# Kernel tuning notes

Measured on AMD Instinct MI355X. Metric: run time of the kernel, lower is better.

Reference implementation:

```python
import jax, jax.numpy as jnp
import numpy as np

THETA = 10000.0
H, D_NOPE, D_ROPE, D_V = 12, 64, 64, 128
D_MODEL, D_LAT = 768, 128
B, S = 4, 2048


def _rope(x, pos, theta=THETA):
    # x: (B, S, D) with D even; pos: (S,) int. Matches RoPE.forward exactly
    # (interleaved even/odd rotation, freqs over full flattened D).
    D = x.shape[-1]
    inv_freq = 1.0 / theta ** (jnp.arange(0, D, 2, dtype=jnp.float32) / D)
    ang = pos.astype(jnp.float32)[:, None] * inv_freq        # (S, D/2)
    c, s = jnp.cos(ang), jnp.sin(ang)
    xe, xo = x[..., 0::2], x[..., 1::2]
    out = jnp.stack([xe * c - xo * s, xe * s + xo * c], axis=-1)
    return out.reshape(x.shape)


def setup_inputs() -> dict:
    key = jax.random.key(0)
    ks = jax.random.split(key, 12)
    std = 0.02
    inp = {
        'x': jax.random.normal(ks[0], (B, S, D_MODEL), jnp.float32),
        'token_positions': jnp.arange(S, dtype=jnp.int64) if jax.config.jax_enable_x64 else jnp.arange(S, dtype=jnp.int32),
        'W_dkv': jax.random.normal(ks[1], (D_LAT, D_MODEL), jnp.float32) * std,
        'b_dkv': jnp.zeros((D_LAT,), jnp.float32),
        'W_dq': jax.random.normal(ks[2], (D_LAT, D_MODEL), jnp.float32) * std,
        'b_dq': jnp.zeros((D_LAT,), jnp.float32),
        'W_uk_nope': jax.random.normal(ks[3], (H * D_NOPE, D_LAT), jnp.float32) * std,
        'b_uk_nope': jnp.zeros((H * D_NOPE,), jnp.float32),
        'W_uv': jax.random.normal(ks[4], (H * D_V, D_LAT), jnp.float32) * std,
        'b_uv': jnp.zeros((H * D_V,), jnp.float32),
        'W_uq_nope': jax.random.normal(ks[5], (H * D_NOPE, D_LAT), jnp.float32) * std,
        'b_uq_nope': jnp.zeros((H * D_NOPE,), jnp.float32),
        'W_uq_rope': jax.random.normal(ks[6], (H * D_ROPE, D_LAT), jnp.float32) * std,
        'b_uq_rope': jnp.zeros((H * D_ROPE,), jnp.float32),
        'W_uk_rope': jax.random.normal(ks[7], (H * D_ROPE, D_MODEL), jnp.float32) * std,
        'b_uk_rope': jnp.zeros((H * D_ROPE,), jnp.float32),
        'W_o': jax.random.normal(ks[8], (D_MODEL, H * D_V), jnp.float32) * std,
        'b_o': jnp.zeros((D_MODEL,), jnp.float32),
    }
    return inp


def reference(x, token_positions, W_dkv, b_dkv, W_dq, b_dq,
              W_uk_nope, b_uk_nope, W_uv, b_uv, W_uq_nope, b_uq_nope,
              W_uq_rope, b_uq_rope, W_uk_rope, b_uk_rope, W_o, b_o):
    b, s, _ = x.shape
    lin = lambda t, W, bb: t @ W.T + bb
    d_qk = D_NOPE + D_ROPE  # 128

    C_kv = lin(x, W_dkv, b_dkv)               # (B,S,128)
    C_q = lin(x, W_dq, b_dq)                  # (B,S,128)

    q_nope = lin(C_q, W_uq_nope, b_uq_nope)   # (B,S,H*64)
    k_nope = lin(C_kv, W_uk_nope, b_uk_nope)  # (B,S,H*64)
    v = lin(C_kv, W_uv, b_uv)                 # (B,S,H*128)

    q_rope = _rope(lin(C_q, W_uq_rope, b_uq_rope), token_positions)
    k_rope = _rope(lin(x, W_uk_rope, b_uk_rope), token_positions)

    # Faithful to torch: concat flattened nope||rope then view into heads.
    q = jnp.concatenate([q_nope, q_rope], axis=-1).reshape(b, s, H, d_qk).transpose(0, 2, 1, 3)
    k = jnp.concatenate([k_nope, k_rope], axis=-1).reshape(b, s, H, d_qk).transpose(0, 2, 1, 3)
    vh = v.reshape(b, s, H, D_V).transpose(0, 2, 1, 3)

    scale = 1.0 / jnp.sqrt(jnp.asarray(d_qk, x.dtype))
    logits = jnp.einsum('bhqd,bhkd->bhqk', q, k) * scale
    causal = jnp.tril(jnp.ones((s, s), bool))
    logits = jnp.where(causal, logits, jnp.finfo(logits.dtype).min)
    attn = jax.nn.softmax(logits, axis=-1)
    o = jnp.einsum('bhqk,bhkd->bhqd', attn, vh)      # (B,H,S,Dv)
    o = o.transpose(0, 2, 1, 3).reshape(b, s, H * D_V)
    return o @ W_o.T + b_o
```

## Files before the change

kernel.cpp:

```cpp
#include <hip/hip_runtime.h>

typedef __attribute__((ext_vector_type(8))) short short8;
typedef __attribute__((ext_vector_type(4))) short short4v;
typedef __attribute__((ext_vector_type(2))) int int2v;
typedef __attribute__((ext_vector_type(4))) float float4v;

#define MFMA16(a, b, c) __builtin_amdgcn_mfma_f32_16x16x32_bf16((a), (b), (c), 0, 0, 0)

__device__ __forceinline__ short f2bf(float f) {
  unsigned u = __float_as_uint(f);
  u += 0x7fffu + ((u >> 16) & 1u);
  return (short)(u >> 16);
}

__device__ __forceinline__ int pkbf(float a, float b) {
  return (int)(unsigned short)f2bf(a) | (((int)(unsigned short)f2bf(b)) << 16);
}

__device__ __forceinline__ int cvtpk(float a, float b) {
  int r;
  asm("v_cvt_pk_bf16_f32 %0, %1, %2" : "=v"(r) : "v"(a), "v"(b));
  return r;
}

__device__ __forceinline__ void glds16(const short* g, short* l) {
  __builtin_amdgcn_global_load_lds(
      (const __attribute__((address_space(1))) void*)g,
      (__attribute__((address_space(3))) void*)l, 16, 0, 0);
}

struct CastSeg { const float* src; short* dst; int n4; };
struct CastArgs { CastSeg seg[9]; int start[10]; };

__global__ __launch_bounds__(256) void castk(CastArgs a) {
  int blk = blockIdx.x;
  int si = 0;
#pragma unroll
  for (int i = 1; i < 9; i++) si += (blk >= a.start[i]);
  int i = (blk - a.start[si]) * 256 + threadIdx.x;
  if (i >= a.seg[si].n4) return;
  float4v f = ((const float4v*)a.seg[si].src)[i];
  short4v o;
  o[0] = f2bf(f[0]); o[1] = f2bf(f[1]); o[2] = f2bf(f[2]); o[3] = f2bf(f[3]);
  ((short4v*)a.seg[si].dst)[i] = o;
}

template <int ROPE, int OUTMODE, int SCALE>
__global__ __launch_bounds__(256, 2) void gemm_t(
    const short* __restrict__ A, int lda, const short* __restrict__ W, int ldw,
    const float* __restrict__ bias0, const float* __restrict__ bias1,
    int bsplit, int ropestart, void* __restrict__ outp, int ldo, int ocol,
    int K, const int* __restrict__ pos) {
  int tid = threadIdx.x, w = tid >> 6, lane = tid & 63;
  int quad = lane >> 4, l16 = lane & 15;
  int bm = blockIdx.y * 128, bn = blockIdx.x * 128;
  int wm = (w & 1) * 64, wn = (w >> 1) * 64;

  __shared__ short At[2][128 * 64];
  __shared__ short Bt[2][128 * 64];

  int srow[4], soff[4];
#pragma unroll
  for (int j = 0; j < 4; j++) {
    int r = w * 32 + j * 8 + (lane >> 3);
    srow[j] = r;
    soff[j] = ((lane & 7) ^ (r & 7)) << 3;
  }
  const short* Ag = A + (size_t)bm * lda;
  const short* Wg = W + (size_t)bn * ldw;

#pragma unroll
  for (int j = 0; j < 4; j++)
    glds16(Ag + (size_t)srow[j] * lda + soff[j], &At[0][(w * 32 + j * 8) * 64]);
#pragma unroll
  for (int j = 0; j < 4; j++)
    glds16(Wg + (size_t)srow[j] * ldw + soff[j], &Bt[0][(w * 32 + j * 8) * 64]);

  float4v acc[4][4];
  float4v z = {0.f, 0.f, 0.f, 0.f};
#pragma unroll
  for (int mi = 0; mi < 4; mi++)
#pragma unroll
    for (int ni = 0; ni < 4; ni++) acc[mi][ni] = z;

  int nk = K >> 6;
  for (int it = 0; it < nk; it++) {
    __syncthreads();
    if (it + 1 < nk) {
      int kt = (it + 1) << 6, nb = (it + 1) & 1;
#pragma unroll
      for (int j = 0; j < 4; j++)
        glds16(Ag + (size_t)srow[j] * lda + kt + soff[j],
               &At[nb][(w * 32 + j * 8) * 64]);
#pragma unroll
      for (int j = 0; j < 4; j++)
        glds16(Wg + (size_t)srow[j] * ldw + kt + soff[j],
               &Bt[nb][(w * 32 + j * 8) * 64]);
    }
    const short* Ab = At[it & 1];
    const short* Bb = Bt[it & 1];
#pragma unroll
    for (int ks = 0; ks < 2; ks++) {
      short8 af[4], bf[4];
#pragma unroll
      for (int mi = 0; mi < 4; mi++) {
        int row = wm + mi * 16 + l16;
        af[mi] = *(const short8*)&Ab[(row << 6) + ((((ks << 2) + quad) ^ (row & 7)) << 3)];
      }
#pragma unroll
      for (int ni = 0; ni < 4; ni++) {
        int row = wn + ni * 16 + l16;
        bf[ni] = *(const short8*)&Bb[(row << 6) + ((((ks << 2) + quad) ^ (row & 7)) << 3)];
      }
#pragma unroll
      for (int mi = 0; mi < 4; mi++)
#pragma unroll
        for (int ni = 0; ni < 4; ni++)
          acc[mi][ni] = MFMA16(af[mi], bf[ni], acc[mi][ni]);
    }
  }

#pragma unroll
  for (int ni = 0; ni < 4; ni++) {
    int col = bn + wn + ni * 16 + l16;
    float bv = (col < bsplit) ? bias0[col] : bias1[col - bsplit];
    float fr = 0.f;
    bool dorope = ROPE && (col >= ropestart);
    if (dorope) {
      int ri = (col - ropestart) & ~1;
      fr = exp2f((float)ri * (-13.287712379549449f / 768.0f));
    }
#pragma unroll
    for (int mi = 0; mi < 4; mi++) {
      int row0 = bm + wm + mi * 16 + quad * 4;
      if (OUTMODE == 2) {
        int bidx = row0 >> 11, s = row0 & 2047;
        short4v ov;
#pragma unroll
        for (int r = 0; r < 4; r++) ov[r] = f2bf(acc[mi][ni][r] + bv);
        *(short4v*)((short*)outp + ((size_t)(bidx * 1536 + col)) * 2048 + s) = ov;
      } else {
#pragma unroll
        for (int r = 0; r < 4; r++) {
          int row = row0 + r;
          float v = acc[mi][ni][r] + bv;
          if (ROPE) {
            float pv = __shfl_xor(v, 1, 64);
            if (dorope) {
              float ang = (float)pos[row & 2047] * fr;
              float sn, cs;
              __sincosf(ang, &sn, &cs);
              v = (col & 1) ? (pv * sn + v * cs) : (v * cs - pv * sn);
            }
          }
          if (SCALE) v *= 0.12751743f;
          if (OUTMODE == 1)
            ((float*)outp)[(size_t)row * ldo + ocol + col] = v;
          else
            ((short*)outp)[(size_t)row * ldo + ocol + col] = f2bf(v);
        }
      }
    }
  }
}

__global__ __launch_bounds__(256, 2) void mla_attn(const short* __restrict__ Q,
                                                   const short* __restrict__ K,
                                                   const short* __restrict__ Vt,
                                                   short* __restrict__ O) {
  const int ld = 1536, SEQ = 2048;
  int tid = threadIdx.x, w = tid >> 6, lane = tid & 63;
  int quad = lane >> 4, l16 = lane & 15;
  int o = (int)blockIdx.x;
  int rank = o / 48;
  int g = o - rank * 48;
  int qt = (15 - rank) * 128;
  int hh = g % 12, b = g / 12;
  int qw = qt + w * 32;

  __shared__ short Kt[2][64 * 128];
  __shared__ short Vl[2][128 * 64];
  __shared__ short Pm[4][32 * 64];
  short* pw = Pm[w];

  int kgo[4], vgo[4];
#pragma unroll
  for (int j = 0; j < 4; j++) {
    int rk = (w * 4 + j) * 4 + (lane >> 4);
    kgo[j] = rk * ld + (((lane & 15) ^ (rk & 7)) << 3);
    int rv = (w * 4 + j) * 8 + (lane >> 3);
    vgo[j] = rv * SEQ + (((lane & 7) ^ (rv & 7)) << 3);
  }
  const short* Kg = K + (size_t)b * SEQ * ld + hh * 128;
  const short* Vg = Vt + (size_t)(b * 12 + hh) * 128 * SEQ;

  short8 qf[2][4];
  {
    const short* Qg = Q + (size_t)(b * SEQ + qw + l16) * ld + hh * 128 + quad * 8;
#pragma unroll
    for (int nf = 0; nf < 2; nf++)
#pragma unroll
      for (int ks = 0; ks < 4; ks++)
        qf[nf][ks] = *(const short8*)(Qg + (size_t)nf * 16 * ld + ks * 32);
  }

  float4v z = {0.f, 0.f, 0.f, 0.f};
  float4v oacc[2][8];
#pragma unroll
  for (int mq = 0; mq < 2; mq++)
#pragma unroll
    for (int df = 0; df < 8; df++) oacc[mq][df] = z;
  float l_i[2] = {0.f, 0.f};

#pragma unroll
  for (int j = 0; j < 4; j++) glds16(Kg + kgo[j], &Kt[0][(w * 4 + j) * 512]);
#pragma unroll
  for (int j = 0; j < 4; j++) glds16(Vg + vgo[j], &Vl[0][(w * 4 + j) * 512]);

  int ntiles = (qt >> 6) + 2;
  for (int it = 0; it < ntiles; it++) {
    int kt = it << 6;
    __syncthreads();
    if (it + 1 < ntiles) {
      int nb = (it + 1) & 1;
      const short* kn = Kg + (size_t)(kt + 64) * ld;
      const short* vn = Vg + (kt + 64);
#pragma unroll
      for (int j = 0; j < 4; j++) glds16(kn + kgo[j], &Kt[nb][(w * 4 + j) * 512]);
#pragma unroll
      for (int j = 0; j < 4; j++) glds16(vn + vgo[j], &Vl[nb][(w * 4 + j) * 512]);
    }
    if (kt > qw + 31) continue;
    const short* Kb = Kt[it & 1];
    const short* Vb = Vl[it & 1];

    float4v sf[4][2];
#pragma unroll
    for (int mf = 0; mf < 4; mf++)
#pragma unroll
      for (int nf = 0; nf < 2; nf++) sf[mf][nf] = z;
    __builtin_amdgcn_s_setprio(1);
#pragma unroll
    for (int ks = 0; ks < 4; ks++)
#pragma unroll
      for (int mf = 0; mf < 4; mf++) {
        int row = mf * 16 + l16;
        short8 a = *(const short8*)&Kb[(row << 7) + (((ks * 4 + quad) ^ (row & 7)) << 3)];
#pragma unroll
        for (int nf = 0; nf < 2; nf++) sf[mf][nf] = MFMA16(a, qf[nf][ks], sf[mf][nf]);
      }
    __builtin_amdgcn_s_setprio(0);
    if (kt + 63 > qw) {
#pragma unroll
      for (int mf = 0; mf < 4; mf++) {
        int key = kt + mf * 16 + quad * 4;
#pragma unroll
        for (int nf = 0; nf < 2; nf++) {
          int q = qw + nf * 16 + l16;
#pragma unroll
          for (int r = 0; r < 4; r++)
            if (key + r > q) sf[mf][nf][r] = -3e38f;
        }
      }
    }
#pragma unroll
    for (int nf = 0; nf < 2; nf++) {
      float ps = 0.f;
#pragma unroll
      for (int mf = 0; mf < 4; mf++)
#pragma unroll
        for (int r = 0; r < 4; r++) {
          float e = exp2f(sf[mf][nf][r]);
          sf[mf][nf][r] = e;
          ps += e;
        }
      l_i[nf] += ps;
#pragma unroll
      for (int mf = 0; mf < 4; mf++) {
        int2v pk;
        pk[0] = cvtpk(sf[mf][nf][0], sf[mf][nf][1]);
        pk[1] = cvtpk(sf[mf][nf][2], sf[mf][nf][3]);
        int p = (mf * 2 + (quad >> 1)) ^ (l16 & 7);
        *(int2v*)&pw[((nf * 16 + l16) << 6) + (p << 3) + ((quad & 1) << 2)] = pk;
      }
    }
    __builtin_amdgcn_s_setprio(1);
#pragma unroll
    for (int t = 0; t < 2; t++) {
      short8 pf[2];
#pragma unroll
      for (int mq = 0; mq < 2; mq++)
        pf[mq] = *(const short8*)&pw[((mq * 16 + l16) << 6) +
                                     ((((t << 2) + quad) ^ (l16 & 7)) << 3)];
#pragma unroll
      for (int df = 0; df < 8; df++) {
        int vr = df * 16 + l16;
        short8 vf = *(const short8*)&Vb[(vr << 6) + ((((t << 2) + quad) ^ (vr & 7)) << 3)];
#pragma unroll
        for (int mq = 0; mq < 2; mq++) oacc[mq][df] = MFMA16(pf[mq], vf, oacc[mq][df]);
      }
    }
    __builtin_amdgcn_s_setprio(0);
  }

  short* Og = O + (size_t)(b * SEQ + qw) * ld + hh * 128;
#pragma unroll
  for (int mq = 0; mq < 2; mq++) {
    float l = l_i[mq];
    l += __shfl_xor(l, 16, 64);
    l += __shfl_xor(l, 32, 64);
    float linv = 1.0f / l;
    float lb[4];
#pragma unroll
    for (int r = 0; r < 4; r++) lb[r] = __shfl(linv, (quad << 2) + r, 64);
#pragma unroll
    for (int df = 0; df < 8; df++)
#pragma unroll
      for (int r = 0; r < 4; r++)
        Og[(size_t)(mq * 16 + (quad << 2) + r) * ld + df * 16 + l16] =
            f2bf(oacc[mq][df][r] * lb[r]);
  }
}

extern "C" void kernel_launch(void* const* d_in, const int* in_sizes, int n_in,
                              void* d_out, int out_size, void* d_ws, size_t ws_size,
                              hipStream_t stream) {
  const int S = 2048, DM = 768, DL = 128, HD = 1536;
  const int M = 4 * S;
  const int BIG = 1 << 28;

  const float* x = (const float*)d_in[0];
  const int* pos = (const int*)d_in[1];
  const float* W_dkv = (const float*)d_in[2];
  const float* b_dkv = (const float*)d_in[3];
  const float* W_dq = (const float*)d_in[4];
  const float* b_dq = (const float*)d_in[5];
  const float* W_uk_nope = (const float*)d_in[6];
  const float* b_uk_nope = (const float*)d_in[7];
  const float* W_uv = (const float*)d_in[8];
  const float* b_uv = (const float*)d_in[9];
  const float* W_uq_nope = (const float*)d_in[10];
  const float* b_uq_nope = (const float*)d_in[11];
  const float* W_uq_rope = (const float*)d_in[12];
  const float* b_uq_rope = (const float*)d_in[13];
  const float* W_uk_rope = (const float*)d_in[14];
  const float* b_uk_rope = (const float*)d_in[15];
  const float* W_o = (const float*)d_in[16];
  const float* b_o = (const float*)d_in[17];

  char* p = (char*)d_ws;
  size_t off = 0;
  auto take = [&](size_t nelem) -> short* {
    short* r = (short*)(p + off);
    off += (nelem * 2 + 255) & ~(size_t)255;
    return r;
  };
  short* xb = take((size_t)M * DM);
  short* Wdq = take(DL * DM);
  short* Wdkv = take(DL * DM);
  short* Wuqnope = take(768 * DL);
  short* Wuqrope = take(768 * DL);
  short* Wuknope = take(768 * DL);
  short* Wuv = take(1536 * DL);
  short* Wukrope = take(768 * DM);
  short* Wo = take(768 * 1536);
  short* Cm = take((size_t)M * 256);
  short* Qm = take((size_t)M * HD);
  short* Km = take((size_t)M * HD);
  short* Vtm = take((size_t)M * HD);
  short* Om = take((size_t)M * HD);
  if (off > ws_size) return;

  CastArgs ca;
  const float* srcs[9] = {x, W_dq, W_dkv, W_uq_nope, W_uq_rope, W_uk_nope, W_uv, W_uk_rope, W_o};
  short* dsts[9] = {xb, Wdq, Wdkv, Wuqnope, Wuqrope, Wuknope, Wuv, Wukrope, Wo};
  int ns[9] = {M * DM, DL * DM, DL * DM, 768 * DL, 768 * DL, 768 * DL, 1536 * DL, 768 * DM, 768 * 1536};
  ca.start[0] = 0;
  for (int i = 0; i < 9; i++) {
    ca.seg[i].src = srcs[i];
    ca.seg[i].dst = dsts[i];
    ca.seg[i].n4 = ns[i] / 4;
    ca.start[i + 1] = ca.start[i] + (ca.seg[i].n4 + 255) / 256;
  }
  castk<<<dim3(ca.start[9]), dim3(256), 0, stream>>>(ca);

  gemm_t<0, 0, 0><<<dim3(2, M / 128), dim3(256), 0, stream>>>(
      xb, DM, Wdq, DM, b_dq, b_dkv, 128, 0, Cm, 256, 0, DM, pos);
  gemm_t<1, 0, 1><<<dim3(12, M / 128), dim3(256), 0, stream>>>(
      Cm, 256, Wuqnope, DL, b_uq_nope, b_uq_rope, 768, 768, Qm, HD, 0, DL, pos);
  gemm_t<0, 0, 0><<<dim3(6, M / 128), dim3(256), 0, stream>>>(
      Cm + 128, 256, Wuknope, DL, b_uk_nope, b_uk_nope, BIG, 0, Km, HD, 0, DL, pos);
  gemm_t<1, 0, 0><<<dim3(6, M / 128), dim3(256), 0, stream>>>(
      xb, DM, Wukrope, DM, b_uk_rope, b_uk_rope, BIG, 0, Km, HD, 768, DM, pos);
  gemm_t<0, 2, 0><<<dim3(12, M / 128), dim3(256), 0, stream>>>(
      Cm + 128, 256, Wuv, DL, b_uv, b_uv, BIG, 0, Vtm, 0, 0, DL, pos);
  mla_attn<<<dim3(768), dim3(256), 0, stream>>>(Qm, Km, Vtm, Om);
  gemm_t<0, 1, 0><<<dim3(6, M / 128), dim3(256), 0, stream>>>(
      Om, HD, Wo, HD, b_o, b_o, BIG, 0, d_out, 768, 0, HD, pos);
}
```

Baseline: 326.5 us.

## Batch projection GEMMs into grouped launches and unroll attention tile loop

Replaces the templated GEMM with a runtime-dispatched grouped GEMM, so independent projections share one launch each: down-projections plus k_rope, and q/k_nope/v up-projections. For K=128 it loads both K tiles up front and syncs once. The attention loop is unrolled by two with static buffer indices and precomputed LDS byte offsets. The aim is fewer launches, better wave fill and less address arithmetic, at the cost of runtime flag branches and higher register pressure in the epilogue.

```diff
diff --git a/kernel.cpp b/kernel.cpp
--- a/kernel.cpp
+++ b/kernel.cpp
@@ -11,10 +11,6 @@
   unsigned u = __float_as_uint(f);
   u += 0x7fffu + ((u >> 16) & 1u);
   return (short)(u >> 16);
-}
-
-__device__ __forceinline__ int pkbf(float a, float b) {
-  return (int)(unsigned short)f2bf(a) | (((int)(unsigned short)f2bf(b)) << 16);
 }
 
 __device__ __forceinline__ int cvtpk(float a, float b) {
@@ -45,16 +41,25 @@
   ((short4v*)a.seg[si].dst)[i] = o;
 }
 
-template <int ROPE, int OUTMODE, int SCALE>
-__global__ __launch_bounds__(256, 2) void gemm_t(
-    const short* __restrict__ A, int lda, const short* __restrict__ W, int ldw,
-    const float* __restrict__ bias0, const float* __restrict__ bias1,
-    int bsplit, int ropestart, void* __restrict__ outp, int ldo, int ocol,
-    int K, const int* __restrict__ pos) {
+struct GSeg {
+  const short* A;
+  const short* W;
+  const float* bias0;
+  const float* bias1;
+  void* outp;
+  int lda, ldw, bsplit, ropestart, ldo, ocol, K, flags;
+};
+struct GArgs { GSeg s[3]; int start[4]; };
+
+__global__ __launch_bounds__(256, 2) void gemm_rt(GArgs ga, const int* __restrict__ pos) {
+  int bx = blockIdx.x;
+  int si = (bx >= ga.start[1]) + (bx >= ga.start[2]);
+  const GSeg sg = ga.s[si];
   int tid = threadIdx.x, w = tid >> 6, lane = tid & 63;
   int quad = lane >> 4, l16 = lane & 15;
-  int bm = blockIdx.y * 128, bn = blockIdx.x * 128;
+  int bm = blockIdx.y * 128, bn = (bx - ga.start[si]) * 128;
   int wm = (w & 1) * 64, wn = (w >> 1) * 64;
+  int lda = sg.lda, ldw = sg.ldw;
 
   __shared__ short At[2][128 * 64];
   __shared__ short Bt[2][128 * 64];
@@ -66,15 +71,8 @@
     srow[j] = r;
     soff[j] = ((lane & 7) ^ (r & 7)) << 3;
   }
-  const short* Ag = A + (size_t)bm * lda;
-  const short* Wg = W + (size_t)bn * ldw;
-
-#pragma unroll
-  for (int j = 0; j < 4; j++)
-    glds16(Ag + (size_t)srow[j] * lda + soff[j], &At[0][(w * 32 + j * 8) * 64]);
-#pragma unroll
-  for (int j = 0; j < 4; j++)
-    glds16(Wg + (size_t)srow[j] * ldw + soff[j], &Bt[0][(w * 32 + j * 8) * 64]);
+  const short* Ag = sg.A + (size_t)bm * lda;
+  const short* Wg = sg.W + (size_t)bn * ldw;
 
   float4v acc[4][4];
   float4v z = {0.f, 0.f, 0.f, 0.f};
@@ -83,22 +81,7 @@
 #pragma unroll
     for (int ni = 0; ni < 4; ni++) acc[mi][ni] = z;
 
-  int nk = K >> 6;
-  for (int it = 0; it < nk; it++) {
-    __syncthreads();
-    if (it + 1 < nk) {
-      int kt = (it + 1) << 6, nb = (it + 1) & 1;
-#pragma unroll
-      for (int j = 0; j < 4; j++)
-        glds16(Ag + (size_t)srow[j] * lda + kt + soff[j],
-               &At[nb][(w * 32 + j * 8) * 64]);
-#pragma unroll
-      for (int j = 0; j < 4; j++)
-        glds16(Wg + (size_t)srow[j] * ldw + kt + soff[j],
-               &Bt[nb][(w * 32 + j * 8) * 64]);
-    }
-    const short* Ab = At[it & 1];
-    const short* Bb = Bt[it & 1];
+  auto comp = [&](const short* Ab, const short* Bb) {
 #pragma unroll
     for (int ks = 0; ks < 2; ks++) {
       short8 af[4], bf[4];
@@ -118,33 +101,71 @@
         for (int ni = 0; ni < 4; ni++)
           acc[mi][ni] = MFMA16(af[mi], bf[ni], acc[mi][ni]);
     }
-  }
-
+  };
+
+  int nk = sg.K >> 6;
+  if (nk == 2) {
+#pragma unroll
+    for (int j = 0; j < 4; j++) {
+      glds16(Ag + (size_t)srow[j] * lda + soff[j], &At[0][(w * 32 + j * 8) * 64]);
+      glds16(Ag + (size_t)srow[j] * lda + 64 + soff[j], &At[1][(w * 32 + j * 8) * 64]);
+      glds16(Wg + (size_t)srow[j] * ldw + soff[j], &Bt[0][(w * 32 + j * 8) * 64]);
+      glds16(Wg + (size_t)srow[j] * ldw + 64 + soff[j], &Bt[1][(w * 32 + j * 8) * 64]);
+    }
+    __syncthreads();
+    comp(At[0], Bt[0]);
+    comp(At[1], Bt[1]);
+  } else {
+#pragma unroll
+    for (int j = 0; j < 4; j++)
+      glds16(Ag + (size_t)srow[j] * lda + soff[j], &At[0][(w * 32 + j * 8) * 64]);
+#pragma unroll
+    for (int j = 0; j < 4; j++)
+      glds16(Wg + (size_t)srow[j] * ldw + soff[j], &Bt[0][(w * 32 + j * 8) * 64]);
+    for (int it = 0; it < nk; it++) {
+      __syncthreads();
+      if (it + 1 < nk) {
+        int kt = (it + 1) << 6, nb = (it + 1) & 1;
+#pragma unroll
+        for (int j = 0; j < 4; j++)
+          glds16(Ag + (size_t)srow[j] * lda + kt + soff[j],
+                 &At[nb][(w * 32 + j * 8) * 64]);
+#pragma unroll
+        for (int j = 0; j < 4; j++)
+          glds16(Wg + (size_t)srow[j] * ldw + kt + soff[j],
+                 &Bt[nb][(w * 32 + j * 8) * 64]);
+      }
+      comp(At[it & 1], Bt[it & 1]);
+    }
+  }
+
+  bool ropeF = sg.flags & 1, scaleF = sg.flags & 2;
+  bool vtF = sg.flags & 4, f32F = sg.flags & 8;
 #pragma unroll
   for (int ni = 0; ni < 4; ni++) {
     int col = bn + wn + ni * 16 + l16;
-    float bv = (col < bsplit) ? bias0[col] : bias1[col - bsplit];
+    float bv = (col < sg.bsplit) ? sg.bias0[col] : sg.bias1[col - sg.bsplit];
     float fr = 0.f;
-    bool dorope = ROPE && (col >= ropestart);
+    bool dorope = ropeF && (col >= sg.ropestart);
     if (dorope) {
-      int ri = (col - ropestart) & ~1;
+      int ri = (col - sg.ropestart) & ~1;
       fr = exp2f((float)ri * (-13.287712379549449f / 768.0f));
     }
 #pragma unroll
     for (int mi = 0; mi < 4; mi++) {
       int row0 = bm + wm + mi * 16 + quad * 4;
-      if (OUTMODE == 2) {
+      if (vtF) {
         int bidx = row0 >> 11, s = row0 & 2047;
         short4v ov;
 #pragma unroll
         for (int r = 0; r < 4; r++) ov[r] = f2bf(acc[mi][ni][r] + bv);
-        *(short4v*)((short*)outp + ((size_t)(bidx * 1536 + col)) * 2048 + s) = ov;
+        *(short4v*)((short*)sg.outp + ((size_t)(bidx * 1536 + col)) * 2048 + s) = ov;
       } else {
 #pragma unroll
         for (int r = 0; r < 4; r++) {
           int row = row0 + r;
           float v = acc[mi][ni][r] + bv;
-          if (ROPE) {
+          if (ropeF) {
             float pv = __shfl_xor(v, 1, 64);
             if (dorope) {
               float ang = (float)pos[row & 2047] * fr;
@@ -153,11 +174,11 @@
               v = (col & 1) ? (pv * sn + v * cs) : (v * cs - pv * sn);
             }
           }
-          if (SCALE) v *= 0.12751743f;
-          if (OUTMODE == 1)
-            ((float*)outp)[(size_t)row * ldo + ocol + col] = v;
+          if (scaleF) v *= 0.12751743f;
+          if (f32F)
+            ((float*)sg.outp)[(size_t)row * sg.ldo + sg.ocol + col] = v;
           else
-            ((short*)outp)[(size_t)row * ldo + ocol + col] = f2bf(v);
+            ((short*)sg.outp)[(size_t)row * sg.ldo + sg.ocol + col] = f2bf(v);
         }
       }
     }
@@ -181,7 +202,7 @@
   __shared__ short Kt[2][64 * 128];
   __shared__ short Vl[2][128 * 64];
   __shared__ short Pm[4][32 * 64];
-  short* pw = Pm[w];
+  char* pwB = (char*)Pm[w];
 
   int kgo[4], vgo[4];
 #pragma unroll
@@ -204,6 +225,31 @@
         qf[nf][ks] = *(const short8*)(Qg + (size_t)nf * 16 * ld + ks * 32);
   }
 
+  int koff[4][4], voff[2][8], pfo[2][2], pwo[2][4];
+#pragma unroll
+  for (int ks = 0; ks < 4; ks++)
+#pragma unroll
+    for (int mf = 0; mf < 4; mf++) {
+      int row = mf * 16 + l16;
+      koff[ks][mf] = row * 256 + ((((ks << 2) + quad) ^ (row & 7)) << 4);
+    }
+#pragma unroll
+  for (int t = 0; t < 2; t++) {
+#pragma unroll
+    for (int df = 0; df < 8; df++) {
+      int vr = df * 16 + l16;
+      voff[t][df] = vr * 128 + ((((t << 2) + quad) ^ (vr & 7)) << 4);
+    }
+#pragma unroll
+    for (int mq = 0; mq < 2; mq++)
+      pfo[t][mq] = (mq * 16 + l16) * 128 + ((((t << 2) + quad) ^ (l16 & 7)) << 4);
+#pragma unroll
+    for (int mf = 0; mf < 4; mf++) {
+      int p = (mf * 2 + (quad >> 1)) ^ (l16 & 7);
+      pwo[t][mf] = (t * 16 + l16) * 128 + (p << 4) + ((quad & 1) << 3);
+    }
+  }
+
   float4v z = {0.f, 0.f, 0.f, 0.f};
   float4v oacc[2][8];
 #pragma unroll
@@ -218,90 +264,82 @@
   for (int j = 0; j < 4; j++) glds16(Vg + vgo[j], &Vl[0][(w * 4 + j) * 512]);
 
   int ntiles = (qt >> 6) + 2;
-  for (int it = 0; it < ntiles; it++) {
-    int kt = it << 6;
-    __syncthreads();
-    if (it + 1 < ntiles) {
-      int nb = (it + 1) & 1;
-      const short* kn = Kg + (size_t)(kt + 64) * ld;
-      const short* vn = Vg + (kt + 64);
-#pragma unroll
-      for (int j = 0; j < 4; j++) glds16(kn + kgo[j], &Kt[nb][(w * 4 + j) * 512]);
-#pragma unroll
-      for (int j = 0; j < 4; j++) glds16(vn + vgo[j], &Vl[nb][(w * 4 + j) * 512]);
-    }
-    if (kt > qw + 31) continue;
-    const short* Kb = Kt[it & 1];
-    const short* Vb = Vl[it & 1];
-
-    float4v sf[4][2];
-#pragma unroll
-    for (int mf = 0; mf < 4; mf++)
-#pragma unroll
-      for (int nf = 0; nf < 2; nf++) sf[mf][nf] = z;
-    __builtin_amdgcn_s_setprio(1);
-#pragma unroll
-    for (int ks = 0; ks < 4; ks++)
-#pragma unroll
-      for (int mf = 0; mf < 4; mf++) {
-        int row = mf * 16 + l16;
-        short8 a = *(const short8*)&Kb[(row << 7) + (((ks * 4 + quad) ^ (row & 7)) << 3)];
-#pragma unroll
-        for (int nf = 0; nf < 2; nf++) sf[mf][nf] = MFMA16(a, qf[nf][ks], sf[mf][nf]);
-      }
-    __builtin_amdgcn_s_setprio(0);
-    if (kt + 63 > qw) {
-#pragma unroll
-      for (int mf = 0; mf < 4; mf++) {
-        int key = kt + mf * 16 + quad * 4;
-#pragma unroll
-        for (int nf = 0; nf < 2; nf++) {
-          int q = qw + nf * 16 + l16;
-#pragma unroll
-          for (int r = 0; r < 4; r++)
-            if (key + r > q) sf[mf][nf][r] = -3e38f;
-        }
-      }
-    }
-#pragma unroll
-    for (int nf = 0; nf < 2; nf++) {
-      float ps = 0.f;
-#pragma unroll
-      for (int mf = 0; mf < 4; mf++)
-#pragma unroll
-        for (int r = 0; r < 4; r++) {
-          float e = exp2f(sf[mf][nf][r]);
-          sf[mf][nf][r] = e;
-          ps += e;
-        }
-      l_i[nf] += ps;
-#pragma unroll
-      for (int mf = 0; mf < 4; mf++) {
-        int2v pk;
-        pk[0] = cvtpk(sf[mf][nf][0], sf[mf][nf][1]);
-        pk[1] = cvtpk(sf[mf][nf][2], sf[mf][nf][3]);
-        int p = (mf * 2 + (quad >> 1)) ^ (l16 & 7);
-        *(int2v*)&pw[((nf * 16 + l16) << 6) + (p << 3) + ((quad & 1) << 2)] = pk;
-      }
-    }
-    __builtin_amdgcn_s_setprio(1);
-#pragma unroll
-    for (int t = 0; t < 2; t++) {
-      short8 pf[2];
-#pragma unroll
-      for (int mq = 0; mq < 2; mq++)
-        pf[mq] = *(const short8*)&pw[((mq * 16 + l16) << 6) +
-                                     ((((t << 2) + quad) ^ (l16 & 7)) << 3)];
-#pragma unroll
-      for (int df = 0; df < 8; df++) {
-        int vr = df * 16 + l16;
-        short8 vf = *(const short8*)&Vb[(vr << 6) + ((((t << 2) + quad) ^ (vr & 7)) << 3)];
-#pragma unroll
-        for (int mq = 0; mq < 2; mq++) oacc[mq][df] = MFMA16(pf[mq], vf, oacc[mq][df]);
-      }
-    }
-    __builtin_amdgcn_s_setprio(0);
-  }
+
+#define ATTN_TILE(IT, NB, NB1)                                                 \
+  do {                                                                         \
+    int kt = (IT) << 6;                                                        \
+    __syncthreads();                                                           \
+    if ((IT) + 1 < ntiles) {                                                   \
+      const short* kn = Kg + (size_t)(kt + 64) * ld;                           \
+      const short* vn = Vg + (kt + 64);                                        \
+      _Pragma("unroll") for (int j = 0; j < 4; j++)                            \
+          glds16(kn + kgo[j], &Kt[NB1][(w * 4 + j) * 512]);                    \
+      _Pragma("unroll") for (int j = 0; j < 4; j++)                            \
+          glds16(vn + vgo[j], &Vl[NB1][(w * 4 + j) * 512]);                    \
+    }                                                                          \
+    if (kt <= qw + 31) {                                                       \
+      const char* Kb = (const char*)Kt[NB];                                    \
+      const char* Vb = (const char*)Vl[NB];                                    \
+      float4v sf[4][2];                                                        \
+      __builtin_amdgcn_s_setprio(1);                                           \
+      _Pragma("unroll") for (int mf = 0; mf < 4; mf++) {                       \
+        short8 a = *(const short8*)(Kb + koff[0][mf]);                         \
+        sf[mf][0] = MFMA16(a, qf[0][0], z);                                    \
+        sf[mf][1] = MFMA16(a, qf[1][0], z);                                    \
+      }                                                                        \
+      _Pragma("unroll") for (int ks = 1; ks < 4; ks++) {                       \
+        _Pragma("unroll") for (int mf = 0; mf < 4; mf++) {                     \
+          short8 a = *(const short8*)(Kb + koff[ks][mf]);                      \
+          sf[mf][0] = MFMA16(a, qf[0][ks], sf[mf][0]);                         \
+          sf[mf][1] = MFMA16(a, qf[1][ks], sf[mf][1]);                         \
+        }                                                                      \
+      }                                                                        \
+      __builtin_amdgcn_s_setprio(0);                                           \
+      if (kt + 63 > qw) {                                                      \
+        _Pragma("unroll") for (int mf = 0; mf < 4; mf++) {                     \
+          int key = kt + mf * 16 + quad * 4;                                   \
+          _Pragma("unroll") for (int nf = 0; nf < 2; nf++) {                   \
+            int q = qw + nf * 16 + l16;                                        \
+            _Pragma("unroll") for (int r = 0; r < 4; r++)                      \
+                if (key + r > q) sf[mf][nf][r] = -3e38f;                       \
+          }                                                                    \
+        }                                                                      \
+      }                                                                        \
+      _Pragma("unroll") for (int nf = 0; nf < 2; nf++) {                       \
+        float ps = 0.f;                                                        \
+        _Pragma("unroll") for (int mf = 0; mf < 4; mf++)                       \
+            _Pragma("unroll") for (int r = 0; r < 4; r++) {                    \
+          float e = exp2f(sf[mf][nf][r]);                                      \
+          sf[mf][nf][r] = e;                                                   \
+          ps += e;                                                             \
+        }                                                                      \
+        l_i[nf] += ps;                                                         \
+        _Pragma("unroll") for (int mf = 0; mf < 4; mf++) {                     \
+          int2v pk;                                                            \
+          pk[0] = cvtpk(sf[mf][nf][0], sf[mf][nf][1]);                         \
+          pk[1] = cvtpk(sf[mf][nf][2], sf[mf][nf][3]);                         \
+          *(int2v*)(pwB + pwo[nf][mf]) = pk;                                   \
+        }                                                                      \
+      }                                                                        \
+      __builtin_amdgcn_s_setprio(1);                                           \
+      _Pragma("unroll") for (int t = 0; t < 2; t++) {                          \
+        short8 pf0 = *(const short8*)(pwB + pfo[t][0]);                        \
+        short8 pf1 = *(const short8*)(pwB + pfo[t][1]);                        \
+        _Pragma("unroll") for (int df = 0; df < 8; df++) {                     \
+          short8 vf = *(const short8*)(Vb + voff[t][df]);                      \
+          oacc[0][df] = MFMA16(pf0, vf, oacc[0][df]);                          \
+          oacc[1][df] = MFMA16(pf1, vf, oacc[1][df]);                          \
+        }                                                                      \
+      }                                                                        \
+      __builtin_amdgcn_s_setprio(0);                                           \
+    }                                                                          \
+  } while (0)
+
+  for (int it = 0; it < ntiles; it += 2) {
+    ATTN_TILE(it, 0, 1);
+    ATTN_TILE(it + 1, 1, 0);
+  }
+#undef ATTN_TILE
 
   short* Og = O + (size_t)(b * SEQ + qw) * ld + hh * 128;
 #pragma unroll
@@ -384,17 +422,38 @@
   }
   castk<<<dim3(ca.start[9]), dim3(256), 0, stream>>>(ca);
 
-  gemm_t<0, 0, 0><<<dim3(2, M / 128), dim3(256), 0, stream>>>(
-      xb, DM, Wdq, DM, b_dq, b_dkv, 128, 0, Cm, 256, 0, DM, pos);
-  gemm_t<1, 0, 1><<<dim3(12, M / 128), dim3(256), 0, stream>>>(
-      Cm, 256, Wuqnope, DL, b_uq_nope, b_uq_rope, 768, 768, Qm, HD, 0, DL, pos);
-  gemm_t<0, 0, 0><<<dim3(6, M / 128), dim3(256), 0, stream>>>(
-      Cm + 128, 256, Wuknope, DL, b_uk_nope, b_uk_nope, BIG, 0, Km, HD, 0, DL, pos);
-  gemm_t<1, 0, 0><<<dim3(6, M / 128), dim3(256), 0, stream>>>(
-      xb, DM, Wukrope, DM, b_uk_rope, b_uk_rope, BIG, 0, Km, HD, 768, DM, pos);
-  gemm_t<0, 2, 0><<<dim3(12, M / 128), dim3(256), 0, stream>>>(
-      Cm + 128, 256, Wuv, DL, b_uv, b_uv, BIG, 0, Vtm, 0, 0, DL, pos);
+  GArgs g1;
+  g1.s[0].A = xb;   g1.s[0].W = Wdq;      g1.s[0].bias0 = b_dq;      g1.s[0].bias1 = b_dkv;
+  g1.s[0].outp = Cm; g1.s[0].lda = DM; g1.s[0].ldw = DM; g1.s[0].bsplit = 128;
+  g1.s[0].ropestart = 0; g1.s[0].ldo = 256; g1.s[0].ocol = 0; g1.s[0].K = DM; g1.s[0].flags = 0;
+  g1.s[1].A = xb;   g1.s[1].W = Wukrope;  g1.s[1].bias0 = b_uk_rope; g1.s[1].bias1 = b_uk_rope;
+  g1.s[1].outp = Km; g1.s[1].lda = DM; g1.s[1].ldw = DM; g1.s[1].bsplit = BIG;
+  g1.s[1].ropestart = 0; g1.s[1].ldo = HD; g1.s[1].ocol = 768; g1.s[1].K = DM; g1.s[1].flags = 1;
+  g1.s[2] = g1.s[1];
+  g1.start[0] = 0; g1.start[1] = 2; g1.start[2] = 8; g1.start[3] = 8;
+  gemm_rt<<<dim3(8, M / 128), dim3(256), 0, stream>>>(g1, pos);
+
+  GArgs g2;
+  g2.s[0].A = Cm;   g2.s[0].W = Wuqnope;  g2.s[0].bias0 = b_uq_nope; g2.s[0].bias1 = b_uq_rope;
+  g2.s[0].outp = Qm; g2.s[0].lda = 256; g2.s[0].ldw = DL; g2.s[0].bsplit = 768;
+  g2.s[0].ropestart = 768; g2.s[0].ldo = HD; g2.s[0].ocol = 0; g2.s[0].K = DL; g2.s[0].flags = 1 | 2;
+  g2.s[1].A = Cm + 128; g2.s[1].W = Wuknope; g2.s[1].bias0 = b_uk_nope; g2.s[1].bias1 = b_uk_nope;
+  g2.s[1].outp = Km; g2.s[1].lda = 256; g2.s[1].ldw = DL; g2.s[1].bsplit = BIG;
+  g2.s[1].ropestart = 0; g2.s[1].ldo = HD; g2.s[1].ocol = 0; g2.s[1].K = DL; g2.s[1].flags = 0;
+  g2.s[2].A = Cm + 128; g2.s[2].W = Wuv;   g2.s[2].bias0 = b_uv;      g2.s[2].bias1 = b_uv;
+  g2.s[2].outp = Vtm; g2.s[2].lda = 256; g2.s[2].ldw = DL; g2.s[2].bsplit = BIG;
+  g2.s[2].ropestart = 0; g2.s[2].ldo = 0; g2.s[2].ocol = 0; g2.s[2].K = DL; g2.s[2].flags = 4;
+  g2.start[0] = 0; g2.start[1] = 12; g2.start[2] = 18; g2.start[3] = 30;
+  gemm_rt<<<dim3(30, M / 128), dim3(256), 0, stream>>>(g2, pos);
+
   mla_attn<<<dim3(768), dim3(256), 0, stream>>>(Qm, Km, Vtm, Om);
-  gemm_t<0, 1, 0><<<dim3(6, M / 128), dim3(256), 0, stream>>>(
-      Om, HD, Wo, HD, b_o, b_o, BIG, 0, d_out, 768, 0, HD, pos);
-}
+
+  GArgs g3;
+  g3.s[0].A = Om;   g3.s[0].W = Wo;       g3.s[0].bias0 = b_o;       g3.s[0].bias1 = b_o;
+  g3.s[0].outp = d_out; g3.s[0].lda = HD; g3.s[0].ldw = HD; g3.s[0].bsplit = BIG;
+  g3.s[0].ropestart = 0; g3.s[0].ldo = 768; g3.s[0].ocol = 0; g3.s[0].K = HD; g3.s[0].flags = 8;
+  g3.s[1] = g3.s[0];
+  g3.s[2] = g3.s[0];
+  g3.start[0] = 0; g3.start[1] = 6; g3.start[2] = 6; g3.start[3] = 6;
+  gemm_rt<<<dim3(6, M / 128), dim3(256), 0, stream>>>(g3, pos);
+}
```

Measured after the change: 311.0 us. -4.7%, faster.
